# Optimization experiments

Measured on AMD Instinct MI355X. Metric: run time of the kernel, lower is better.

## Reference

```python
import jax, jax.numpy as jnp
import numpy as np

N_NODES = 100000
N_EDGES = 1600000
IN_DIM = 128
OUT_DIM = 128
NEG_SLOPE = 0.2


def setup_inputs() -> dict:
    key = jax.random.key(0)
    ks = jax.random.split(key, 7)
    x = jax.random.normal(ks[0], (N_NODES, IN_DIM), dtype=jnp.float32)
    edge_index = jax.random.randint(ks[1], (2, N_EDGES), 0, N_NODES, dtype=jnp.int32)
    # xavier-ish scale for [in, out] weight layout (y = x @ W)
    s = float(np.sqrt(2.0 / (IN_DIM + OUT_DIM)))
    W_q = jax.random.normal(ks[2], (IN_DIM, OUT_DIM), dtype=jnp.float32) * s
    W_k = jax.random.normal(ks[3], (IN_DIM, OUT_DIM), dtype=jnp.float32) * s
    W_v = jax.random.normal(ks[4], (IN_DIM, OUT_DIM), dtype=jnp.float32) * s
    W_l = jax.random.normal(ks[5], (IN_DIM, OUT_DIM), dtype=jnp.float32) * s
    b_l = jnp.zeros((OUT_DIM,), dtype=jnp.float32)
    return {"x": x, "edge_index": edge_index, "W_q": W_q, "W_k": W_k,
            "W_v": W_v, "W_l": W_l, "b_l": b_l}


def reference(x, edge_index, W_q, W_k, W_v, W_l, b_l):
    num_nodes = x.shape[0]
    row, col = edge_index[0], edge_index[1]

    h_q = x @ W_q                                   # [N, D]
    h_k = x @ W_k                                   # [N, D]
    _h_v = x @ W_v                                  # computed in original, unused downstream

    # aggregated query: sum of neighbor queries per destination node
    q_agg = jax.ops.segment_sum(h_q[col], row, num_segments=num_nodes)  # [N, D]
    k_act = jax.nn.leaky_relu(h_k, NEG_SLOPE)

    # per-edge attention scores (note: original uses raw q_agg, not activated)
    scores = jnp.sum(k_act[row] * q_agg[col], axis=1) / (OUT_DIM ** 0.5)  # [E]

    # scatter-softmax over edges grouped by destination (row)
    max_val = jax.ops.segment_max(scores, row, num_segments=num_nodes)
    exp_scores = jnp.exp(scores - max_val[row])
    sum_exp = jax.ops.segment_sum(exp_scores, row, num_segments=num_nodes)
    alpha = exp_scores / (sum_exp[row] + 1e-8)      # [E]; dropout is identity in eval

    h_proj = x @ W_l + b_l                          # [N, D]
    weighted = alpha[:, None] * h_proj[col]         # [E, D]
    h_prime = jax.ops.segment_sum(weighted, row, num_segments=num_nodes)
    return jax.nn.leaky_relu(h_prime, NEG_SLOPE)
```

## Files before the change

kernel.cpp:

```cpp
#include <hip/hip_runtime.h>
#include <math.h>

#define N_NODES 100000
#define N_EDGES 1600000
#define DIM 128
#define CAP 64

#define NB1 196
#define NPB 512
#define CHUNK1 4096
#define GRID1 391
#define SLOT1 52
#define LSTRIDE 197

typedef short bf16x8 __attribute__((ext_vector_type(8)));
typedef float f32x4 __attribute__((ext_vector_type(4)));

static __device__ __forceinline__ unsigned bf16rne(float f) {
    unsigned u = __float_as_uint(f);
    return (u + 0x7FFFu + ((u >> 16) & 1u)) >> 16;
}
static __device__ __forceinline__ float bflo(unsigned u) { return __uint_as_float(u << 16); }
static __device__ __forceinline__ float bfhi(unsigned u) { return __uint_as_float(u & 0xFFFF0000u); }


__global__ __launch_bounds__(256) void pb_k(
    const float* __restrict__ x, const float* __restrict__ Wq,
    const float* __restrict__ Wk, const float* __restrict__ Wl,
    const int* __restrict__ row, const int* __restrict__ col,
    ushort* __restrict__ xb, ushort* __restrict__ kq,
    ushort* __restrict__ WlTh, ushort* __restrict__ WlTl,
    unsigned* __restrict__ bkt, int* __restrict__ bktc) {
    __shared__ uint4 smem4[4352];
    int j = blockIdx.x, t = threadIdx.x;

    if (j % 3 == 2) {
        int blk = j / 3;
        int* lcnt = (int*)smem4;
        unsigned* lbuf = (unsigned*)smem4 + 256;
        if (t < NB1) lcnt[t] = 0;
        __syncthreads();
        long base = (long)blk * CHUNK1;
        if (base + CHUNK1 <= N_EDGES) {
            const uint4* r4 = (const uint4*)row + (size_t)blk * 1024;
            const uint4* c4 = (const uint4*)col + (size_t)blk * 1024;
#pragma unroll
            for (int q = 0; q < 4; q++) {
                uint4 rv = r4[q * 256 + t];
                uint4 cv = c4[q * 256 + t];
                unsigned rr[4] = {rv.x, rv.y, rv.z, rv.w};
                unsigned cc[4] = {cv.x, cv.y, cv.z, cv.w};
#pragma unroll
                for (int i = 0; i < 4; i++) {
                    int b = rr[i] >> 9;
                    int p = atomicAdd(&lcnt[b], 1);
                    if (p < SLOT1) lbuf[p * LSTRIDE + b] = (cc[i] << 9) | (rr[i] & 511u);
                }
            }
        } else {
            for (int i = t; base + i < N_EDGES; i += 256) {
                unsigned r = (unsigned)row[base + i], c = (unsigned)col[base + i];
                int b = r >> 9;
                int p = atomicAdd(&lcnt[b], 1);
                if (p < SLOT1) lbuf[p * LSTRIDE + b] = (c << 9) | (r & 511u);
            }
        }
        __syncthreads();
        if (t < NB1) bktc[(size_t)blk * NB1 + t] = min(lcnt[t], SLOT1);
        int wave = t >> 6, lane = t & 63;
        for (int s = wave; s < NB1; s += 4) {
            if (lane < min(lcnt[s], SLOT1))
                bkt[((size_t)s * GRID1 + blk) * SLOT1 + lane] = lbuf[lane * LSTRIDE + s];
        }
        return;
    }

    int p = (j / 3) * 2 + (j % 3);
    ushort* b1 = (ushort*)smem4;
    ushort* b2 = b1 + 17408;

    if (p == 0) {
        for (int i = t; i < 16384; i += 256) {
            int k = i >> 7, n = i & 127;
            float v = Wl[i];
            unsigned hi = bf16rne(v);
            WlTh[n * 128 + k] = (ushort)hi;
            WlTl[n * 128 + k] = (ushort)bf16rne(v - bflo(hi));
        }
    }
    for (int i = t; i < 16384; i += 256) {
        int k = i >> 7, n = i & 127;
        b2[n * 136 + k] = (ushort)bf16rne(Wk[i]);
    }

    int wave = t >> 6, lane = t & 63;
    int ln15 = lane & 15, quad = lane >> 4;
    long base = (long)p * 128 + wave * 32;

    bf16x8 Af[2][4];
#pragma unroll
    for (int r = 0; r < 2; r++) {
        long rw = base + r * 16 + ln15;
        long rowc = rw < N_NODES ? rw : N_NODES - 1;
#pragma unroll
        for (int s = 0; s < 4; s++) {
            int ch = s * 4 + quad;
            const float4* xp = (const float4*)(x + rowc * 128 + ch * 8);
            float4 u0 = xp[0], u1 = xp[1];
            bf16x8 f;
            f[0] = (short)bf16rne(u0.x); f[1] = (short)bf16rne(u0.y);
            f[2] = (short)bf16rne(u0.z); f[3] = (short)bf16rne(u0.w);
            f[4] = (short)bf16rne(u1.x); f[5] = (short)bf16rne(u1.y);
            f[6] = (short)bf16rne(u1.z); f[7] = (short)bf16rne(u1.w);
            Af[r][s] = f;
            if (rw < N_NODES) *(bf16x8*)(xb + rw * 128 + ch * 8) = f;
        }
    }
    f32x4 acc[2][8];
#pragma unroll
    for (int r = 0; r < 2; r++)
#pragma unroll
        for (int t8 = 0; t8 < 8; t8++) acc[r][t8] = (f32x4){0.f, 0.f, 0.f, 0.f};

    __syncthreads();
#pragma unroll
    for (int s = 0; s < 4; s++) {
#pragma unroll
        for (int t8 = 0; t8 < 8; t8++) {
            bf16x8 b = *(const bf16x8*)(b2 + (t8 * 16 + ln15) * 136 + (s * 4 + quad) * 8);
            acc[0][t8] = __builtin_amdgcn_mfma_f32_16x16x32_bf16(Af[0][s], b, acc[0][t8], 0, 0, 0);
            acc[1][t8] = __builtin_amdgcn_mfma_f32_16x16x32_bf16(Af[1][s], b, acc[1][t8], 0, 0, 0);
        }
    }
    __syncthreads();
    for (int i = t; i < 16384; i += 256) {
        int k = i >> 7, n = i & 127;
        float v = Wk[i];
        unsigned hi = bf16rne(v);
        b2[n * 136 + k] = (ushort)bf16rne(v - bflo(hi));
    }
    __syncthreads();
#pragma unroll
    for (int s = 0; s < 4; s++) {
#pragma unroll
        for (int t8 = 0; t8 < 8; t8++) {
            bf16x8 b = *(const bf16x8*)(b2 + (t8 * 16 + ln15) * 136 + (s * 4 + quad) * 8);
            acc[0][t8] = __builtin_amdgcn_mfma_f32_16x16x32_bf16(Af[0][s], b, acc[0][t8], 0, 0, 0);
            acc[1][t8] = __builtin_amdgcn_mfma_f32_16x16x32_bf16(Af[1][s], b, acc[1][t8], 0, 0, 0);
        }
    }
#pragma unroll
    for (int r = 0; r < 2; r++) {
#pragma unroll
        for (int reg = 0; reg < 4; reg++) {
            int rl = wave * 32 + r * 16 + quad * 4 + reg;
#pragma unroll
            for (int t8 = 0; t8 < 8; t8++) {
                float v = acc[r][t8][reg];
                v = v > 0.f ? v : 0.2f * v;
                b1[rl * 136 + t8 * 16 + ln15] = (ushort)bf16rne(v);
            }
        }
    }
    __syncthreads();
    for (int i = t; i < 16384; i += 256) {
        b2[(i >> 7) * 136 + (i & 127)] = (ushort)bf16rne(Wq[i]);
    }
    __syncthreads();
#pragma unroll
    for (int r = 0; r < 2; r++)
#pragma unroll
        for (int t8 = 0; t8 < 8; t8++) acc[r][t8] = (f32x4){0.f, 0.f, 0.f, 0.f};
#pragma unroll
    for (int r = 0; r < 2; r++) {
        bf16x8 af[4];
#pragma unroll
        for (int s = 0; s < 4; s++)
            af[s] = *(const bf16x8*)(b1 + (wave * 32 + r * 16 + ln15) * 136 + (s * 4 + quad) * 8);
#pragma unroll
        for (int s = 0; s < 4; s++) {
#pragma unroll
            for (int t8 = 0; t8 < 8; t8++) {
                bf16x8 b = *(const bf16x8*)(b2 + (t8 * 16 + ln15) * 136 + (s * 4 + quad) * 8);
                acc[r][t8] = __builtin_amdgcn_mfma_f32_16x16x32_bf16(af[s], b, acc[r][t8], 0, 0, 0);
            }
        }
    }
    __syncthreads();
    for (int i = t; i < 16384; i += 256) {
        float v = Wq[i];
        unsigned hi = bf16rne(v);
        b2[(i >> 7) * 136 + (i & 127)] = (ushort)bf16rne(v - bflo(hi));
    }
    __syncthreads();
#pragma unroll
    for (int r = 0; r < 2; r++) {
        bf16x8 af[4];
#pragma unroll
        for (int s = 0; s < 4; s++)
            af[s] = *(const bf16x8*)(b1 + (wave * 32 + r * 16 + ln15) * 136 + (s * 4 + quad) * 8);
#pragma unroll
        for (int s = 0; s < 4; s++) {
#pragma unroll
            for (int t8 = 0; t8 < 8; t8++) {
                bf16x8 b = *(const bf16x8*)(b2 + (t8 * 16 + ln15) * 136 + (s * 4 + quad) * 8);
                acc[r][t8] = __builtin_amdgcn_mfma_f32_16x16x32_bf16(af[s], b, acc[r][t8], 0, 0, 0);
            }
        }
    }
#pragma unroll
    for (int r = 0; r < 2; r++) {
#pragma unroll
        for (int reg = 0; reg < 4; reg++) {
            long node = base + r * 16 + quad * 4 + reg;
            if (node < N_NODES) {
#pragma unroll
                for (int t8 = 0; t8 < 8; t8++)
                    kq[node * 128 + t8 * 16 + ln15] = (ushort)bf16rne(acc[r][t8][reg]);
            }
        }
    }
}


__global__ __launch_bounds__(1024) void build_k(const int* __restrict__ bktc,
                                                const unsigned* __restrict__ bkt,
                                                int* __restrict__ cur,
                                                int* __restrict__ scol) {
    __shared__ int lcur[NPB];
    __shared__ int lc[GRID1];
    int b = blockIdx.x, t = threadIdx.x;
    if (t < NPB) lcur[t] = 0;
    if (t < GRID1) lc[t] = bktc[(size_t)t * NB1 + b];
    __syncthreads();
    int wave = t >> 6, lane = t & 63;
    const unsigned* D = bkt + (size_t)b * GRID1 * SLOT1;
    for (int s = wave; s < GRID1; s += 16) {
        if (lane < lc[s]) {
            unsigned v = D[(size_t)s * SLOT1 + lane];
            int rl = (int)(v & 511u);
            int c = (int)(v >> 9);
            int p = atomicAdd(&lcur[rl], 1);
            if (p < CAP) scol[((size_t)b * NPB + rl) * CAP + p] = c;
        }
    }
    __syncthreads();
    if (t < NPB) {
        int node = b * NPB + t;
        if (node < N_NODES) cur[node] = lcur[t];
    }
}


__global__ __launch_bounds__(256) void xa_k(const uint4* __restrict__ xb4,
                                            const int* __restrict__ cur,
                                            const int* __restrict__ scol,
                                            uint4* __restrict__ ax4) {
    int g = (blockIdx.x * 256 + threadIdx.x) >> 4;
    int gl = threadIdx.x & 15;
    int d = min(cur[g], CAP);
    float a0 = 0.f, a1 = 0.f, a2 = 0.f, a3 = 0.f;
    float a4 = 0.f, a5 = 0.f, a6 = 0.f, a7 = 0.f;
    for (int j = 0; j < d; j += 16) {
        int cb = (j + gl < d) ? scol[(size_t)g * CAP + j + gl] : 0;
        int lim = min(16, d - j);
        int k = 0;
        for (; k + 4 <= lim; k += 4) {
            int c0 = __shfl(cb, k, 16),     c1 = __shfl(cb, k + 1, 16);
            int c2 = __shfl(cb, k + 2, 16), c3 = __shfl(cb, k + 3, 16);
            uint4 u0 = xb4[(size_t)c0 * 16 + gl];
            uint4 u1 = xb4[(size_t)c1 * 16 + gl];
            uint4 u2 = xb4[(size_t)c2 * 16 + gl];
            uint4 u3 = xb4[(size_t)c3 * 16 + gl];
            a0 += bflo(u0.x); a1 += bfhi(u0.x); a2 += bflo(u0.y); a3 += bfhi(u0.y);
            a4 += bflo(u0.z); a5 += bfhi(u0.z); a6 += bflo(u0.w); a7 += bfhi(u0.w);
            a0 += bflo(u1.x); a1 += bfhi(u1.x); a2 += bflo(u1.y); a3 += bfhi(u1.y);
            a4 += bflo(u1.z); a5 += bfhi(u1.z); a6 += bflo(u1.w); a7 += bfhi(u1.w);
            a0 += bflo(u2.x); a1 += bfhi(u2.x); a2 += bflo(u2.y); a3 += bfhi(u2.y);
            a4 += bflo(u2.z); a5 += bfhi(u2.z); a6 += bflo(u2.w); a7 += bfhi(u2.w);
            a0 += bflo(u3.x); a1 += bfhi(u3.x); a2 += bflo(u3.y); a3 += bfhi(u3.y);
            a4 += bflo(u3.z); a5 += bfhi(u3.z); a6 += bflo(u3.w); a7 += bfhi(u3.w);
        }
        for (; k < lim; k++) {
            int c = __shfl(cb, k, 16);
            uint4 u = xb4[(size_t)c * 16 + gl];
            a0 += bflo(u.x); a1 += bfhi(u.x); a2 += bflo(u.y); a3 += bfhi(u.y);
            a4 += bflo(u.z); a5 += bfhi(u.z); a6 += bflo(u.w); a7 += bfhi(u.w);
        }
    }
    uint4 o;
    o.x = bf16rne(a0) | (bf16rne(a1) << 16);
    o.y = bf16rne(a2) | (bf16rne(a3) << 16);
    o.z = bf16rne(a4) | (bf16rne(a5) << 16);
    o.w = bf16rne(a6) | (bf16rne(a7) << 16);
    const uint2* xb2 = (const uint2*)xb4;
    uint2 xp0 = xb2[(size_t)g * 32 + 2 * gl];
    uint2 xp1 = xb2[(size_t)g * 32 + 2 * gl + 1];
    ax4[(size_t)g * 32 + 2 * gl]     = make_uint4(o.x, o.y, xp0.x, xp0.y);
    ax4[(size_t)g * 32 + 2 * gl + 1] = make_uint4(o.z, o.w, xp1.x, xp1.y);
}


__global__ __launch_bounds__(256) void attn_k(const uint2* __restrict__ kq2,
                                              const uint4* __restrict__ ax4,
                                              const int* __restrict__ cur,
                                              const int* __restrict__ scol,
                                              uint2* __restrict__ xwb,
                                              float* __restrict__ sumw) {
    long g = (blockIdx.x * 256 + threadIdx.x) >> 6;
    int lane = threadIdx.x & 63;
    int l31 = lane & 31;
    int h = lane >> 5;
    int d = min(cur[g], CAP);
    uint2 ku = kq2[(size_t)g * 32 + l31];
    const float scale = 0.08838834764831845f;
    float k0 = bflo(ku.x) * scale, k1 = bfhi(ku.x) * scale;
    float k2 = bflo(ku.y) * scale, k3 = bfhi(ku.y) * scale;

    int cb = (lane < d) ? scol[(size_t)g * CAP + lane] : 0;
    float S = 0.f;
    float a0 = 0.f, a1 = 0.f, a2 = 0.f, a3 = 0.f;
    int k = 0;
    for (; k + 8 <= d; k += 8) {
        int c0 = __shfl(cb, k + h, 64);
        int c1 = __shfl(cb, k + 2 + h, 64);
        int c2 = __shfl(cb, k + 4 + h, 64);
        int c3 = __shfl(cb, k + 6 + h, 64);
        uint4 u0 = ax4[(size_t)c0 * 32 + l31];
        uint4 u1 = ax4[(size_t)c1 * 32 + l31];
        uint4 u2 = ax4[(size_t)c2 * 32 + l31];
        uint4 u3 = ax4[(size_t)c3 * 32 + l31];
        float p0 = k0 * bflo(u0.x) + k1 * bfhi(u0.x) + k2 * bflo(u0.y) + k3 * bfhi(u0.y);
        float p1 = k0 * bflo(u1.x) + k1 * bfhi(u1.x) + k2 * bflo(u1.y) + k3 * bfhi(u1.y);
        float p2 = k0 * bflo(u2.x) + k1 * bfhi(u2.x) + k2 * bflo(u2.y) + k3 * bfhi(u2.y);
        float p3 = k0 * bflo(u3.x) + k1 * bfhi(u3.x) + k2 * bflo(u3.y) + k3 * bfhi(u3.y);
#pragma unroll
        for (int off = 16; off > 0; off >>= 1) {
            p0 += __shfl_xor(p0, off, 32); p1 += __shfl_xor(p1, off, 32);
            p2 += __shfl_xor(p2, off, 32); p3 += __shfl_xor(p3, off, 32);
        }
        float e0 = __expf(p0), e1 = __expf(p1);
        float e2 = __expf(p2), e3 = __expf(p3);
        S += (e0 + e1) + (e2 + e3);
        a0 += e0 * bflo(u0.z) + e1 * bflo(u1.z) + e2 * bflo(u2.z) + e3 * bflo(u3.z);
        a1 += e0 * bfhi(u0.z) + e1 * bfhi(u1.z) + e2 * bfhi(u2.z) + e3 * bfhi(u3.z);
        a2 += e0 * bflo(u0.w) + e1 * bflo(u1.w) + e2 * bflo(u2.w) + e3 * bflo(u3.w);
        a3 += e0 * bfhi(u0.w) + e1 * bfhi(u1.w) + e2 * bfhi(u2.w) + e3 * bfhi(u3.w);
    }
    for (; k + 2 <= d; k += 2) {
        int c = __shfl(cb, k + h, 64);
        uint4 u = ax4[(size_t)c * 32 + l31];
        float p = k0 * bflo(u.x) + k1 * bfhi(u.x) + k2 * bflo(u.y) + k3 * bfhi(u.y);
#pragma unroll
        for (int off = 16; off > 0; off >>= 1) p += __shfl_xor(p, off, 32);
        float e0 = __expf(p);
        S += e0;
        a0 += e0 * bflo(u.z);
        a1 += e0 * bfhi(u.z);
        a2 += e0 * bflo(u.w);
        a3 += e0 * bfhi(u.w);
    }
    if (k < d) {
        int c = __shfl(cb, k, 64);
        uint4 u = ax4[(size_t)c * 32 + l31];
        float p = k0 * bflo(u.x) + k1 * bfhi(u.x) + k2 * bflo(u.y) + k3 * bfhi(u.y);
#pragma unroll
        for (int off = 16; off > 0; off >>= 1) p += __shfl_xor(p, off, 32);
        float e0 = __expf(p);
        if (h == 0) {
            S += e0;
            a0 += e0 * bflo(u.z);
            a1 += e0 * bfhi(u.z);
            a2 += e0 * bflo(u.w);
            a3 += e0 * bfhi(u.w);
        }
    }
    S += __shfl_xor(S, 32, 64);
    a0 += __shfl_xor(a0, 32, 64);
    a1 += __shfl_xor(a1, 32, 64);
    a2 += __shfl_xor(a2, 32, 64);
    a3 += __shfl_xor(a3, 32, 64);
    float inv = 1.f / (S + 1e-8f);
    if (h == 0) {
        uint2 o;
        o.x = bf16rne(a0 * inv) | (bf16rne(a1 * inv) << 16);
        o.y = bf16rne(a2 * inv) | (bf16rne(a3 * inv) << 16);
        xwb[(size_t)g * 32 + l31] = o;
        if (l31 == 0) sumw[g] = S * inv;
    }
}


__global__ __launch_bounds__(256) void fin_k(const ushort* __restrict__ Ab,
                                             const ushort* __restrict__ BTh,
                                             const ushort* __restrict__ BTl,
                                             const float* __restrict__ bl,
                                             const float* __restrict__ sumw,
                                             float* __restrict__ out) {
    int tid = threadIdx.x;
    int wave = tid >> 6, lane = tid & 63;
    int ln15 = lane & 15, quad = (lane >> 4) & 3;
    long base = (long)blockIdx.x * 128 + wave * 32;

    const bf16x8* A8 = (const bf16x8*)Ab;
    const bf16x8* Bh8 = (const bf16x8*)BTh;
    const bf16x8* Bl8 = (const bf16x8*)BTl;

    bf16x8 Af[2][4];
#pragma unroll
    for (int r = 0; r < 2; r++) {
        long row = base + r * 16 + ln15;
#pragma unroll
        for (int s = 0; s < 4; s++) Af[r][s] = A8[row * 16 + s * 4 + quad];
    }
    float blv[8];
#pragma unroll
    for (int t = 0; t < 8; t++) blv[t] = bl[t * 16 + ln15];

    f32x4 acc[2][8];
#pragma unroll
    for (int r = 0; r < 2; r++)
#pragma unroll
        for (int t = 0; t < 8; t++) acc[r][t] = (f32x4){0.f, 0.f, 0.f, 0.f};

#pragma unroll
    for (int phase = 0; phase < 2; phase++) {
        const bf16x8* B8 = phase ? Bl8 : Bh8;
#pragma unroll
        for (int s = 0; s < 4; s++) {
#pragma unroll
            for (int t = 0; t < 8; t++) {
                bf16x8 b = B8[(t * 16 + ln15) * 16 + s * 4 + quad];
                acc[0][t] = __builtin_amdgcn_mfma_f32_16x16x32_bf16(Af[0][s], b, acc[0][t], 0, 0, 0);
                acc[1][t] = __builtin_amdgcn_mfma_f32_16x16x32_bf16(Af[1][s], b, acc[1][t], 0, 0, 0);
            }
        }
    }
#pragma unroll
    for (int r = 0; r < 2; r++) {
#pragma unroll
        for (int reg = 0; reg < 4; reg++) {
            long node = base + r * 16 + quad * 4 + reg;
            if (node < N_NODES) {
                float sw = sumw[node];
#pragma unroll
                for (int t = 0; t < 8; t++) {
                    float v = acc[r][t][reg] + sw * blv[t];
                    v = v > 0.f ? v : 0.2f * v;
                    out[node * 128 + t * 16 + ln15] = v;
                }
            }
        }
    }
}


extern "C" void kernel_launch(void* const* d_in, const int* in_sizes, int n_in,
                              void* d_out, int out_size, void* d_ws, size_t ws_size,
                              hipStream_t stream) {
    const float* x  = (const float*)d_in[0];
    const int* row  = (const int*)d_in[1];
    const int* col  = row + N_EDGES;
    const float* Wq = (const float*)d_in[2];
    const float* Wk = (const float*)d_in[3];
    const float* Wl = (const float*)d_in[5];
    const float* bl = (const float*)d_in[6];
    float* out = (float*)d_out;

    ushort* xb    = (ushort*)d_ws;
    ushort* ax    = xb + (size_t)N_NODES * DIM;
    ushort* kq    = ax + (size_t)N_NODES * 256;
    ushort* xwb   = kq + (size_t)N_NODES * DIM;
    ushort* wbuf  = xwb + (size_t)N_NODES * DIM;
    ushort* WlTh = wbuf, *WlTl = wbuf + 16384;
    float* sumw = (float*)(wbuf + 2 * 16384);
    int* cur  = (int*)(sumw + N_NODES);
    int* scol = cur + N_NODES;
    unsigned* bkt = (unsigned*)(scol + (size_t)N_NODES * CAP);
    int* bktc = (int*)(bkt + (size_t)NB1 * GRID1 * SLOT1);

    pb_k<<<1173, 256, 0, stream>>>(x, Wq, Wk, Wl, row, col, xb, kq,
                                   WlTh, WlTl, bkt, bktc);
    build_k<<<NB1, 1024, 0, stream>>>(bktc, bkt, cur, scol);
    xa_k<<<N_NODES / 16, 256, 0, stream>>>((const uint4*)xb, cur, scol, (uint4*)ax);
    attn_k<<<N_NODES / 4, 256, 0, stream>>>((const uint2*)kq, (const uint4*)ax,
                                            cur, scol, (uint2*)xwb, sumw);
    fin_k<<<(N_NODES + 127) / 128, 256, 0, stream>>>(xwb, WlTh, WlTl, bl, sumw, out);
}
```

Measured before the change: 450.2 us.

## Fuse CSR bucket build with neighbor-x aggregation using shared-memory adjacency

Merges the bucket-to-CSR build kernel and the neighbor feature aggregation kernel into one kernel. Each block now handles half a bucket (256 nodes), builds the per-node neighbor lists in LDS, writes them out to global memory for later use, and then aggregates neighbor x rows straight from the LDS list. This removes one launch and the global reread of cur/scol. In exchange, each half-bucket block scans the full bucket data, so bucket reads double. Only 392 blocks of 1024 threads with about 66KB of LDS each run, which may limit how well the gather latency is hidden.

Result: faster. 439.4 us (-2.4%).

```diff
diff --git a/kernel.cpp b/kernel.cpp
--- a/kernel.cpp
+++ b/kernel.cpp
@@ -223,55 +223,64 @@
 }
 
 
-__global__ __launch_bounds__(1024) void build_k(const int* __restrict__ bktc,
-                                                const unsigned* __restrict__ bkt,
-                                                int* __restrict__ cur,
-                                                int* __restrict__ scol) {
-    __shared__ int lcur[NPB];
+__global__ __launch_bounds__(1024) void bxa_k(const int* __restrict__ bktc,
+                                              const unsigned* __restrict__ bkt,
+                                              const uint4* __restrict__ xb4,
+                                              int* __restrict__ cur,
+                                              int* __restrict__ scol,
+                                              uint4* __restrict__ ax4) {
+    __shared__ int lcnt[256];
+    __shared__ int lbkt[256 * CAP];
     __shared__ int lc[GRID1];
-    int b = blockIdx.x, t = threadIdx.x;
-    if (t < NPB) lcur[t] = 0;
+    int blk = blockIdx.x;
+    int b = blk >> 1, half = blk & 1;
+    int t = threadIdx.x;
+    if (t < 256) lcnt[t] = 0;
     if (t < GRID1) lc[t] = bktc[(size_t)t * NB1 + b];
     __syncthreads();
     int wave = t >> 6, lane = t & 63;
     const unsigned* D = bkt + (size_t)b * GRID1 * SLOT1;
+    int hbase = half << 8;
     for (int s = wave; s < GRID1; s += 16) {
         if (lane < lc[s]) {
             unsigned v = D[(size_t)s * SLOT1 + lane];
-            int rl = (int)(v & 511u);
-            int c = (int)(v >> 9);
-            int p = atomicAdd(&lcur[rl], 1);
-            if (p < CAP) scol[((size_t)b * NPB + rl) * CAP + p] = c;
-        }
-    }
-    __syncthreads();
-    if (t < NPB) {
-        int node = b * NPB + t;
-        if (node < N_NODES) cur[node] = lcur[t];
-    }
-}
-
-
-__global__ __launch_bounds__(256) void xa_k(const uint4* __restrict__ xb4,
-                                            const int* __restrict__ cur,
-                                            const int* __restrict__ scol,
-                                            uint4* __restrict__ ax4) {
-    int g = (blockIdx.x * 256 + threadIdx.x) >> 4;
-    int gl = threadIdx.x & 15;
-    int d = min(cur[g], CAP);
-    float a0 = 0.f, a1 = 0.f, a2 = 0.f, a3 = 0.f;
-    float a4 = 0.f, a5 = 0.f, a6 = 0.f, a7 = 0.f;
-    for (int j = 0; j < d; j += 16) {
-        int cb = (j + gl < d) ? scol[(size_t)g * CAP + j + gl] : 0;
-        int lim = min(16, d - j);
+            int rl = (int)(v & 511u) - hbase;
+            if ((unsigned)rl < 256u) {
+                int p = atomicAdd(&lcnt[rl], 1);
+                if (p < CAP) lbkt[rl * CAP + p] = (int)(v >> 9);
+            }
+        }
+    }
+    __syncthreads();
+    long nbase = (long)b * NPB + hbase;
+    int nv = (int)((long)N_NODES - nbase);
+    if (nv > 256) nv = 256;
+    if (nv < 0) nv = 0;
+    if (t < nv) cur[nbase + t] = min(lcnt[t], CAP);
+    {
+        const uint4* lb4 = (const uint4*)lbkt;
+        uint4* sc4 = (uint4*)(scol + nbase * CAP);
+        int qn = nv * (CAP / 4);
+        for (int i = t; i < qn; i += 1024) sc4[i] = lb4[i];
+    }
+    int grp = t >> 4, gl = t & 15;
+    const uint2* xb2 = (const uint2*)xb4;
+#pragma unroll
+    for (int i = 0; i < 4; i++) {
+        int rl = grp * 4 + i;
+        if (rl >= nv) continue;
+        long node = nbase + rl;
+        int d = min(lcnt[rl], CAP);
+        const int* L = &lbkt[rl * CAP];
+        float a0 = 0.f, a1 = 0.f, a2 = 0.f, a3 = 0.f;
+        float a4 = 0.f, a5 = 0.f, a6 = 0.f, a7 = 0.f;
         int k = 0;
-        for (; k + 4 <= lim; k += 4) {
-            int c0 = __shfl(cb, k, 16),     c1 = __shfl(cb, k + 1, 16);
-            int c2 = __shfl(cb, k + 2, 16), c3 = __shfl(cb, k + 3, 16);
-            uint4 u0 = xb4[(size_t)c0 * 16 + gl];
-            uint4 u1 = xb4[(size_t)c1 * 16 + gl];
-            uint4 u2 = xb4[(size_t)c2 * 16 + gl];
-            uint4 u3 = xb4[(size_t)c3 * 16 + gl];
+        for (; k + 4 <= d; k += 4) {
+            int4 cc = *(const int4*)(L + k);
+            uint4 u0 = xb4[(size_t)cc.x * 16 + gl];
+            uint4 u1 = xb4[(size_t)cc.y * 16 + gl];
+            uint4 u2 = xb4[(size_t)cc.z * 16 + gl];
+            uint4 u3 = xb4[(size_t)cc.w * 16 + gl];
             a0 += bflo(u0.x); a1 += bfhi(u0.x); a2 += bflo(u0.y); a3 += bfhi(u0.y);
             a4 += bflo(u0.z); a5 += bfhi(u0.z); a6 += bflo(u0.w); a7 += bfhi(u0.w);
             a0 += bflo(u1.x); a1 += bfhi(u1.x); a2 += bflo(u1.y); a3 += bfhi(u1.y);
@@ -281,23 +290,22 @@
             a0 += bflo(u3.x); a1 += bfhi(u3.x); a2 += bflo(u3.y); a3 += bfhi(u3.y);
             a4 += bflo(u3.z); a5 += bfhi(u3.z); a6 += bflo(u3.w); a7 += bfhi(u3.w);
         }
-        for (; k < lim; k++) {
-            int c = __shfl(cb, k, 16);
+        for (; k < d; k++) {
+            int c = L[k];
             uint4 u = xb4[(size_t)c * 16 + gl];
             a0 += bflo(u.x); a1 += bfhi(u.x); a2 += bflo(u.y); a3 += bfhi(u.y);
             a4 += bflo(u.z); a5 += bfhi(u.z); a6 += bflo(u.w); a7 += bfhi(u.w);
         }
-    }
-    uint4 o;
-    o.x = bf16rne(a0) | (bf16rne(a1) << 16);
-    o.y = bf16rne(a2) | (bf16rne(a3) << 16);
-    o.z = bf16rne(a4) | (bf16rne(a5) << 16);
-    o.w = bf16rne(a6) | (bf16rne(a7) << 16);
-    const uint2* xb2 = (const uint2*)xb4;
-    uint2 xp0 = xb2[(size_t)g * 32 + 2 * gl];
-    uint2 xp1 = xb2[(size_t)g * 32 + 2 * gl + 1];
-    ax4[(size_t)g * 32 + 2 * gl]     = make_uint4(o.x, o.y, xp0.x, xp0.y);
-    ax4[(size_t)g * 32 + 2 * gl + 1] = make_uint4(o.z, o.w, xp1.x, xp1.y);
+        uint4 o;
+        o.x = bf16rne(a0) | (bf16rne(a1) << 16);
+        o.y = bf16rne(a2) | (bf16rne(a3) << 16);
+        o.z = bf16rne(a4) | (bf16rne(a5) << 16);
+        o.w = bf16rne(a6) | (bf16rne(a7) << 16);
+        uint2 xp0 = xb2[(size_t)node * 32 + 2 * gl];
+        uint2 xp1 = xb2[(size_t)node * 32 + 2 * gl + 1];
+        ax4[(size_t)node * 32 + 2 * gl]     = make_uint4(o.x, o.y, xp0.x, xp0.y);
+        ax4[(size_t)node * 32 + 2 * gl + 1] = make_uint4(o.z, o.w, xp1.x, xp1.y);
+    }
 }
 
 
@@ -481,8 +489,8 @@
 
     pb_k<<<1173, 256, 0, stream>>>(x, Wq, Wk, Wl, row, col, xb, kq,
                                    WlTh, WlTl, bkt, bktc);
-    build_k<<<NB1, 1024, 0, stream>>>(bktc, bkt, cur, scol);
-    xa_k<<<N_NODES / 16, 256, 0, stream>>>((const uint4*)xb, cur, scol, (uint4*)ax);
+    bxa_k<<<NB1 * 2, 1024, 0, stream>>>(bktc, bkt, (const uint4*)xb, cur, scol,
+                                        (uint4*)ax);
     attn_k<<<N_NODES / 4, 256, 0, stream>>>((const uint2*)kq, (const uint4*)ax,
                                             cur, scol, (uint2*)xwb, sumw);
     fin_k<<<(N_NODES + 127) / 128, 256, 0, stream>>>(xwb, WlTh, WlTl, bl, sumw, out);
```
